# Kernel tuning notes

Measured on AMD Instinct MI355X. Metric: run time of the kernel, lower is better.

The kernel has to match this reference:

```python
import jax, jax.numpy as jnp
import numpy as np

N = 50000          # nodes
E = 800000         # edges
F_IN = 128         # num_node_features
H = 64             # hidden_channels
G = 64             # graphs in batch
C = 10             # num_classes
L_HID = 3          # num_hidden_layers
EPS = 1e-5


def setup_inputs() -> dict:
    key = jax.random.key(0)
    ks = jax.random.split(key, 16)
    x = jax.random.normal(ks[0], (N, F_IN), dtype=jnp.float32)
    edge_index = jax.random.randint(ks[1], (2, E), 0, N, dtype=jnp.int32)
    batch = jnp.sort(jax.random.randint(ks[2], (N,), 0, G, dtype=jnp.int32))
    s = 0.05
    W_in = jax.random.normal(ks[3], (F_IN, H), dtype=jnp.float32) * s
    b_in = jnp.zeros((H,), dtype=jnp.float32)
    W_hid = jax.random.normal(ks[4], (L_HID, H, H), dtype=jnp.float32) * s
    b_hid = jnp.zeros((L_HID, H), dtype=jnp.float32)
    gamma = jnp.ones((H,), dtype=jnp.float32)
    beta = jnp.zeros((H,), dtype=jnp.float32)
    # MLPReadout: 64 -> 32 -> 16 -> 10
    W1 = jax.random.normal(ks[5], (H, H // 2), dtype=jnp.float32) * s
    b1 = jnp.zeros((H // 2,), dtype=jnp.float32)
    W2 = jax.random.normal(ks[6], (H // 2, H // 4), dtype=jnp.float32) * s
    b2 = jnp.zeros((H // 4,), dtype=jnp.float32)
    W3 = jax.random.normal(ks[7], (H // 4, C), dtype=jnp.float32) * s
    b3 = jnp.zeros((C,), dtype=jnp.float32)
    return {"x": x, "edge_index": edge_index, "batch": batch,
            "W_in": W_in, "b_in": b_in, "W_hid": W_hid, "b_hid": b_hid,
            "gamma": gamma, "beta": beta,
            "W1": W1, "b1": b1, "W2": W2, "b2": b2, "W3": W3, "b3": b3}


def gcn_conv(h_pre, W, b, src, dst, dis):
    # PyG GCNConv with self-loops: out_i = sum_{j->i} d_i^-.5 d_j^-.5 (x_j W) + d_i^-1 (x_i W) + b
    h = h_pre @ W                                   # [N, H]
    norm = (dis[src] * dis[dst])[:, None]           # [E, 1]
    agg = jax.ops.segment_sum(h[src] * norm, dst, num_segments=N)
    agg = agg + h * (dis * dis)[:, None]            # self-loop term
    return agg + b


def batchnorm(x, gamma, beta):
    mu = jnp.mean(x, axis=0)
    var = jnp.mean(jnp.square(x - mu), axis=0)      # biased var (torch BN)
    return (x - mu) * jax.lax.rsqrt(var + EPS) * gamma + beta


def reference(x, edge_index, batch, W_in, b_in, W_hid, b_hid,
              gamma, beta, W1, b1, W2, b2, W3, b3):
    src, dst = edge_index[0], edge_index[1]
    # degree with self-loops (computed on target nodes)
    deg = jax.ops.segment_sum(jnp.ones((E,), x.dtype), dst, num_segments=N) + 1.0
    dis = jax.lax.rsqrt(deg)                        # deg^-0.5

    h = jax.nn.relu(gcn_conv(x, W_in, b_in, src, dst, dis))
    for l in range(L_HID):
        h = gcn_conv(h, W_hid[l], b_hid[l], src, dst, dis)
        h = batchnorm(h, gamma, beta)
        h = jax.nn.relu(h)

    # global mean pool over graphs
    sums = jax.ops.segment_sum(h, batch, num_segments=G)           # [G, H]
    cnts = jax.ops.segment_sum(jnp.ones((N,), x.dtype), batch, num_segments=G)
    pooled = sums / jnp.maximum(cnts, 1.0)[:, None]

    # MLPReadout
    y = jax.nn.relu(pooled @ W1 + b1)
    y = jax.nn.relu(y @ W2 + b2)
    return y @ W3 + b3                               # [G, C]
```

## Files before the change

kernel.cpp:

```cpp
#include <hip/hip_runtime.h>

#define NN 50000
#define NE 800000
#define FIN 128
#define H 64
#define NG 64
#define NC 10
#define EPS 1e-5f
#define NB_SCAN 196
#define GATHER_BLOCKS 12500
#define BNRED_BLOCKS 125

__global__ void count_deg_kernel(const int* __restrict__ dst, int* __restrict__ deg) {
    int e = blockIdx.x * blockDim.x + threadIdx.x;
    if (e < NE) atomicAdd(&deg[dst[e]], 1);
}

__global__ void scan1_kernel(const int* __restrict__ deg, int* __restrict__ ebase,
                             int* __restrict__ bsum, float* __restrict__ dis) {
    __shared__ int s[256];
    int t = threadIdx.x;
    int i = blockIdx.x * 256 + t;
    int v = (i < NN) ? deg[i] : 0;
    if (i < NN) dis[i] = rsqrtf((float)v + 1.0f);
    s[t] = v;
    for (int off = 1; off < 256; off <<= 1) {
        __syncthreads();
        int add = (t >= off) ? s[t - off] : 0;
        __syncthreads();
        s[t] += add;
    }
    __syncthreads();
    if (i < NN) ebase[i] = s[t] - v;
    if (t == 255) bsum[blockIdx.x] = s[255];
}

__global__ void scan2_kernel(int* __restrict__ bsum, const int* __restrict__ batch,
                             int* __restrict__ gstart) {
    int t = threadIdx.x;
    if (t <= NG) {
        int lo = 0, hi = NN;
        while (lo < hi) {
            int mid = (lo + hi) >> 1;
            if (batch[mid] < t) lo = mid + 1; else hi = mid;
        }
        gstart[t] = lo;
    }
    __shared__ int s[256];
    int v = (t < NB_SCAN) ? bsum[t] : 0;
    s[t] = v;
    for (int off = 1; off < 256; off <<= 1) {
        __syncthreads();
        int add = (t >= off) ? s[t - off] : 0;
        __syncthreads();
        s[t] += add;
    }
    __syncthreads();
    if (t < NB_SCAN) bsum[t] = s[t] - v;
}

__global__ void scan3_kernel(int* __restrict__ ebase, const int* __restrict__ bsum) {
    int i = blockIdx.x * blockDim.x + threadIdx.x;
    if (i < NN) ebase[i] += bsum[i >> 8];
    if (i == 0) ebase[NN] = NE;
}

__global__ void fill_kernel(const int* __restrict__ src, const int* __restrict__ dst,
                            const int* __restrict__ ebase, int* __restrict__ cursor,
                            int* __restrict__ eidx) {
    int e = blockIdx.x * blockDim.x + threadIdx.x;
    if (e < NE) {
        int d = dst[e];
        int slot = ebase[d] + atomicAdd(&cursor[d], 1);
        eidx[slot] = src[e];
    }
}

__global__ __launch_bounds__(256, 4) void gemm_fin_kernel(const float* __restrict__ A,
                                                          const float* __restrict__ W,
                                                          const float* __restrict__ dis,
                                                          float* __restrict__ outp) {
    __shared__ float Al[64][65];
    __shared__ float Wl[64 * H];
    const int tid = threadIdx.x;
    const int r0 = blockIdx.x * 64;
    const int row = tid >> 2;
    const int cb  = (tid & 3) << 4;
    float acc[16];
#pragma unroll
    for (int j = 0; j < 16; j++) acc[j] = 0.f;

    for (int k0 = 0; k0 < FIN; k0 += 64) {
        for (int idx = tid; idx < 64 * H; idx += 256) Wl[idx] = W[k0 * H + idx];
        for (int idx = tid; idx < 64 * 64; idx += 256) {
            int r = idx >> 6, c = idx & 63;
            int gr = r0 + r;
            Al[r][c] = (gr < NN) ? A[(long)gr * FIN + k0 + c] : 0.f;
        }
        __syncthreads();
#pragma unroll
        for (int k = 0; k < 64; k++) {
            float a = Al[row][k];
#pragma unroll
            for (int j = 0; j < 16; j++) acc[j] = fmaf(a, Wl[k * H + cb + j], acc[j]);
        }
        __syncthreads();
    }
    int gr = r0 + row;
    if (gr < NN) {
        float ds = dis[gr];
#pragma unroll
        for (int j = 0; j < 16; j++) acc[j] *= ds;
        float4* o = reinterpret_cast<float4*>(&outp[(long)gr * H + cb]);
        o[0] = make_float4(acc[0], acc[1], acc[2], acc[3]);
        o[1] = make_float4(acc[4], acc[5], acc[6], acc[7]);
        o[2] = make_float4(acc[8], acc[9], acc[10], acc[11]);
        o[3] = make_float4(acc[12], acc[13], acc[14], acc[15]);
    }
}

template <int DO_BN>
__global__ __launch_bounds__(256, 4) void gemm_hid_kernel(const float* __restrict__ A,
                                                          const float* __restrict__ W,
                                                          const float* __restrict__ pbn2,
                                                          const float* __restrict__ gamma,
                                                          const float* __restrict__ beta,
                                                          const float* __restrict__ dis,
                                                          float* __restrict__ outp) {
    __shared__ float Al[64][65];
    __shared__ float Wl[64 * H];
    __shared__ float bns[128];
    __shared__ float tot[128];
    const int tid = threadIdx.x;
    if (DO_BN) {
        if (tid < 128) {
            float s = 0.f;
            for (int r = 0; r < BNRED_BLOCKS; ++r) s += pbn2[(long)r * 128 + tid];
            tot[tid] = s;
        }
        __syncthreads();
        if (tid < H) {
            float mu  = tot[tid] * (1.0f / NN);
            float var = tot[H + tid] * (1.0f / NN) - mu * mu;
            float sc  = rsqrtf(var + EPS) * gamma[tid];
            bns[tid]     = sc;
            bns[H + tid] = beta[tid] - mu * sc;
        }
        __syncthreads();
    }
    const int r0 = blockIdx.x * 64;
    const int row = tid >> 2;
    const int cb  = (tid & 3) << 4;
    float acc[16];
#pragma unroll
    for (int j = 0; j < 16; j++) acc[j] = 0.f;

    for (int idx = tid; idx < 64 * H; idx += 256) Wl[idx] = W[idx];
    for (int idx = tid; idx < 64 * 64; idx += 256) {
        int r = idx >> 6, c = idx & 63;
        int gr = r0 + r;
        float a = (gr < NN) ? A[(long)gr * H + c] : 0.f;
        if (DO_BN) a = fmaxf(fmaf(a, bns[c], bns[64 + c]), 0.f);
        Al[r][c] = a;
    }
    __syncthreads();
#pragma unroll
    for (int k = 0; k < 64; k++) {
        float a = Al[row][k];
#pragma unroll
        for (int j = 0; j < 16; j++) acc[j] = fmaf(a, Wl[k * H + cb + j], acc[j]);
    }
    int gr = r0 + row;
    if (gr < NN) {
        float ds = dis[gr];
#pragma unroll
        for (int j = 0; j < 16; j++) acc[j] *= ds;
        float4* o = reinterpret_cast<float4*>(&outp[(long)gr * H + cb]);
        o[0] = make_float4(acc[0], acc[1], acc[2], acc[3]);
        o[1] = make_float4(acc[4], acc[5], acc[6], acc[7]);
        o[2] = make_float4(acc[8], acc[9], acc[10], acc[11]);
        o[3] = make_float4(acc[12], acc[13], acc[14], acc[15]);
    }
}

template <int MODE>
__global__ __launch_bounds__(256) void gather_kernel(const float* __restrict__ hw,
                                                     const int* __restrict__ ebase,
                                                     const int* __restrict__ eidx,
                                                     const float* __restrict__ dis,
                                                     const float* __restrict__ bias,
                                                     float* __restrict__ outp,
                                                     float* __restrict__ pbn) {
    __shared__ float ls[H], lss[H];
    if (MODE == 1) {
        if (threadIdx.x < H) { ls[threadIdx.x] = 0.f; lss[threadIdx.x] = 0.f; }
        __syncthreads();
    }
    const int node = blockIdx.x * 4 + (threadIdx.x >> 6);
    const int lane = threadIdx.x & 63;
    const int grp  = lane >> 4;
    const int c4   = (lane & 15) << 2;
    const int e0 = ebase[node], e1 = ebase[node + 1];
    float4 acc = make_float4(0.f, 0.f, 0.f, 0.f);
    int e = e0 + grp;
    for (; e + 4 < e1; e += 8) {
        int s0 = eidx[e], s1 = eidx[e + 4];
        const float4 v0 = *reinterpret_cast<const float4*>(&hw[(long)s0 * H + c4]);
        const float4 v1 = *reinterpret_cast<const float4*>(&hw[(long)s1 * H + c4]);
        acc.x += v0.x + v1.x;
        acc.y += v0.y + v1.y;
        acc.z += v0.z + v1.z;
        acc.w += v0.w + v1.w;
    }
    if (e < e1) {
        const float4 v0 = *reinterpret_cast<const float4*>(&hw[(long)eidx[e] * H + c4]);
        acc.x += v0.x; acc.y += v0.y; acc.z += v0.z; acc.w += v0.w;
    }
#pragma unroll
    for (int m = 16; m <= 32; m <<= 1) {
        acc.x += __shfl_xor(acc.x, m, 64);
        acc.y += __shfl_xor(acc.y, m, 64);
        acc.z += __shfl_xor(acc.z, m, 64);
        acc.w += __shfl_xor(acc.w, m, 64);
    }
    const float4 self = *reinterpret_cast<const float4*>(&hw[(long)node * H + c4]);
    float ds = dis[node];
    float4 v;
    v.x = fmaf(acc.x + self.x, ds, bias[c4 + 0]);
    v.y = fmaf(acc.y + self.y, ds, bias[c4 + 1]);
    v.z = fmaf(acc.z + self.z, ds, bias[c4 + 2]);
    v.w = fmaf(acc.w + self.w, ds, bias[c4 + 3]);
    if (MODE == 0) {
        v.x = fmaxf(v.x, 0.f); v.y = fmaxf(v.y, 0.f);
        v.z = fmaxf(v.z, 0.f); v.w = fmaxf(v.w, 0.f);
    }
    if (grp == 0) {
        *reinterpret_cast<float4*>(&outp[(long)node * H + c4]) = v;
        if (MODE == 1) {
            atomicAdd(&ls[c4 + 0], v.x); atomicAdd(&lss[c4 + 0], v.x * v.x);
            atomicAdd(&ls[c4 + 1], v.y); atomicAdd(&lss[c4 + 1], v.y * v.y);
            atomicAdd(&ls[c4 + 2], v.z); atomicAdd(&lss[c4 + 2], v.z * v.z);
            atomicAdd(&ls[c4 + 3], v.w); atomicAdd(&lss[c4 + 3], v.w * v.w);
        }
    }
    if (MODE == 1) {
        __syncthreads();
        if (threadIdx.x < H) {
            pbn[(long)blockIdx.x * 128 + threadIdx.x] = ls[threadIdx.x];
            pbn[(long)blockIdx.x * 128 + H + threadIdx.x] = lss[threadIdx.x];
        }
    }
}

__global__ void bnredA_kernel(const float* __restrict__ pbn, float* __restrict__ pbn2) {
    int c = threadIdx.x & 127;
    int half = threadIdx.x >> 7;
    int r0 = blockIdx.x * 100;
    float s = 0.f;
    for (int r = r0 + half; r < r0 + 100; r += 2) s += pbn[(long)r * 128 + c];
    __shared__ float red[256];
    red[threadIdx.x] = s;
    __syncthreads();
    if (half == 0) pbn2[(long)blockIdx.x * 128 + c] = red[c] + red[128 + c];
}

__global__ void pool_mlp_kernel(const float* __restrict__ conv, const float* __restrict__ pbn2,
                                const float* __restrict__ gamma, const float* __restrict__ beta,
                                const int* __restrict__ gstart,
                                const float* __restrict__ W1, const float* __restrict__ b1,
                                const float* __restrict__ W2, const float* __restrict__ b2,
                                const float* __restrict__ W3, const float* __restrict__ b3,
                                float* __restrict__ out) {
    __shared__ float tot[128];
    __shared__ float bns[128];
    __shared__ float red[256];
    __shared__ float pl[H], y1[32], y2[16];
    const int t = threadIdx.x;
    const int g = blockIdx.x;
    if (t < 128) {
        float s = 0.f;
        for (int r = 0; r < BNRED_BLOCKS; ++r) s += pbn2[(long)r * 128 + t];
        tot[t] = s;
    }
    __syncthreads();
    if (t < H) {
        float mu  = tot[t] * (1.0f / NN);
        float var = tot[H + t] * (1.0f / NN) - mu * mu;
        float sc  = rsqrtf(var + EPS) * gamma[t];
        bns[t]     = sc;
        bns[H + t] = beta[t] - mu * sc;
    }
    __syncthreads();
    const int n0 = gstart[g], n1 = gstart[g + 1];
    const int sub = t >> 6, lane = t & 63;
    float sc = bns[lane], sh = bns[H + lane];
    float s = 0.f;
    for (int n = n0 + sub; n < n1; n += 4)
        s += fmaxf(fmaf(conv[(long)n * H + lane], sc, sh), 0.f);
    red[t] = s;
    __syncthreads();
    if (sub == 0) {
        float inv = 1.0f / fmaxf((float)(n1 - n0), 1.0f);
        pl[lane] = (red[lane] + red[64 + lane] + red[128 + lane] + red[192 + lane]) * inv;
    }
    __syncthreads();
    if (t < 32) {
        float v = b1[t];
        for (int k = 0; k < H; k++) v = fmaf(pl[k], W1[k * 32 + t], v);
        y1[t] = fmaxf(v, 0.f);
    }
    __syncthreads();
    if (t < 16) {
        float v = b2[t];
        for (int k = 0; k < 32; k++) v = fmaf(y1[k], W2[k * 16 + t], v);
        y2[t] = fmaxf(v, 0.f);
    }
    __syncthreads();
    if (t < NC) {
        float v = b3[t];
        for (int k = 0; k < 16; k++) v = fmaf(y2[k], W3[k * NC + t], v);
        out[(long)g * NC + t] = v;
    }
}

extern "C" void kernel_launch(void* const* d_in, const int* in_sizes, int n_in,
                              void* d_out, int out_size, void* d_ws, size_t ws_size,
                              hipStream_t stream) {
    const float* x     = (const float*)d_in[0];
    const int*   ei    = (const int*)d_in[1];
    const int*   batch = (const int*)d_in[2];
    const float* W_in  = (const float*)d_in[3];
    const float* b_in  = (const float*)d_in[4];
    const float* W_hid = (const float*)d_in[5];
    const float* b_hid = (const float*)d_in[6];
    const float* gamma = (const float*)d_in[7];
    const float* beta  = (const float*)d_in[8];
    const float* W1    = (const float*)d_in[9];
    const float* b1    = (const float*)d_in[10];
    const float* W2    = (const float*)d_in[11];
    const float* b2    = (const float*)d_in[12];
    const float* W3    = (const float*)d_in[13];
    const float* b3    = (const float*)d_in[14];
    float* out = (float*)d_out;

    const int* src = ei;
    const int* dst = ei + NE;

    int*   deg_i  = (int*)d_ws;
    int*   cursor = deg_i + 50048;
    int*   ebase  = cursor + 50048;
    int*   eidx   = ebase + 50056;
    int*   bsum   = eidx + 800000;
    int*   gstart = bsum + 256;
    float* dis    = (float*)(gstart + 72);
    float* hw     = dis + 50048;
    float* conv   = hw + (long)NN * H;
    float* h      = conv + (long)NN * H;
    float* pbn    = h + (long)NN * H;
    float* pbn2   = pbn + (long)GATHER_BLOCKS * 128;

    const int NB_GEMM = (NN + 63) / 64;
    const int NB_E    = (NE + 255) / 256;
    const int NB_N    = (NN + 255) / 256;

    hipMemsetAsync(deg_i, 0, 2 * 50048 * sizeof(int), stream);
    count_deg_kernel<<<NB_E, 256, 0, stream>>>(dst, deg_i);
    scan1_kernel<<<NB_SCAN, 256, 0, stream>>>(deg_i, ebase, bsum, dis);
    scan2_kernel<<<1, 256, 0, stream>>>(bsum, batch, gstart);
    scan3_kernel<<<NB_N, 256, 0, stream>>>(ebase, bsum);
    fill_kernel<<<NB_E, 256, 0, stream>>>(src, dst, ebase, cursor, eidx);

    gemm_fin_kernel<<<NB_GEMM, 256, 0, stream>>>(x, W_in, dis, hw);
    gather_kernel<0><<<GATHER_BLOCKS, 256, 0, stream>>>(hw, ebase, eidx, dis, b_in, h, nullptr);

    gemm_hid_kernel<0><<<NB_GEMM, 256, 0, stream>>>(h, W_hid, nullptr, nullptr, nullptr, dis, hw);
    gather_kernel<1><<<GATHER_BLOCKS, 256, 0, stream>>>(hw, ebase, eidx, dis, b_hid, conv, pbn);
    bnredA_kernel<<<BNRED_BLOCKS, 256, 0, stream>>>(pbn, pbn2);
    for (int l = 1; l < 3; l++) {
        gemm_hid_kernel<1><<<NB_GEMM, 256, 0, stream>>>(conv, W_hid + (long)l * H * H, pbn2,
                                                        gamma, beta, dis, hw);
        gather_kernel<1><<<GATHER_BLOCKS, 256, 0, stream>>>(hw, ebase, eidx, dis,
                                                            b_hid + (long)l * H, conv, pbn);
        bnredA_kernel<<<BNRED_BLOCKS, 256, 0, stream>>>(pbn, pbn2);
    }

    pool_mlp_kernel<<<NG, 256, 0, stream>>>(conv, pbn2, gamma, beta, gstart,
                                            W1, b1, W2, b2, W3, b3, out);
}
```

Before: 609.7 us.

## Vectorize GEMM tile loads, deepen gather unroll, hoist BN stats, split pooling

GEMM kernels now load the A and W tiles with float4 reads instead of scalar loads. The gather loop is unrolled to four neighbour loads per iteration so more memory requests are in flight. The BatchNorm scale and shift are now computed once per layer in a small bnredB kernel, replacing the 125-row reduction that every GEMM block and every pooling block repeated. Pooling is split across 8 blocks per graph with a second kernel for the MLP, adding launches in exchange for more parallelism.

```diff
diff --git a/kernel.cpp b/kernel.cpp
--- a/kernel.cpp
+++ b/kernel.cpp
@@ -91,11 +91,17 @@
     for (int j = 0; j < 16; j++) acc[j] = 0.f;
 
     for (int k0 = 0; k0 < FIN; k0 += 64) {
-        for (int idx = tid; idx < 64 * H; idx += 256) Wl[idx] = W[k0 * H + idx];
-        for (int idx = tid; idx < 64 * 64; idx += 256) {
-            int r = idx >> 6, c = idx & 63;
+        for (int idx = tid; idx < 64 * 16; idx += 256) {
+            float4 w = *reinterpret_cast<const float4*>(&W[k0 * H + idx * 4]);
+            *reinterpret_cast<float4*>(&Wl[idx * 4]) = w;
+        }
+        for (int idx = tid; idx < 64 * 16; idx += 256) {
+            int r = idx >> 4, c4 = (idx & 15) << 2;
             int gr = r0 + r;
-            Al[r][c] = (gr < NN) ? A[(long)gr * FIN + k0 + c] : 0.f;
+            float4 a = make_float4(0.f, 0.f, 0.f, 0.f);
+            if (gr < NN) a = *reinterpret_cast<const float4*>(&A[(long)gr * FIN + k0 + c4]);
+            Al[r][c4 + 0] = a.x; Al[r][c4 + 1] = a.y;
+            Al[r][c4 + 2] = a.z; Al[r][c4 + 3] = a.w;
         }
         __syncthreads();
 #pragma unroll
@@ -122,30 +128,15 @@
 template <int DO_BN>
 __global__ __launch_bounds__(256, 4) void gemm_hid_kernel(const float* __restrict__ A,
                                                           const float* __restrict__ W,
-                                                          const float* __restrict__ pbn2,
-                                                          const float* __restrict__ gamma,
-                                                          const float* __restrict__ beta,
+                                                          const float* __restrict__ bnsc,
                                                           const float* __restrict__ dis,
                                                           float* __restrict__ outp) {
     __shared__ float Al[64][65];
     __shared__ float Wl[64 * H];
     __shared__ float bns[128];
-    __shared__ float tot[128];
     const int tid = threadIdx.x;
     if (DO_BN) {
-        if (tid < 128) {
-            float s = 0.f;
-            for (int r = 0; r < BNRED_BLOCKS; ++r) s += pbn2[(long)r * 128 + tid];
-            tot[tid] = s;
-        }
-        __syncthreads();
-        if (tid < H) {
-            float mu  = tot[tid] * (1.0f / NN);
-            float var = tot[H + tid] * (1.0f / NN) - mu * mu;
-            float sc  = rsqrtf(var + EPS) * gamma[tid];
-            bns[tid]     = sc;
-            bns[H + tid] = beta[tid] - mu * sc;
-        }
+        if (tid < 128) bns[tid] = bnsc[tid];
         __syncthreads();
     }
     const int r0 = blockIdx.x * 64;
@@ -155,13 +146,23 @@
 #pragma unroll
     for (int j = 0; j < 16; j++) acc[j] = 0.f;
 
-    for (int idx = tid; idx < 64 * H; idx += 256) Wl[idx] = W[idx];
-    for (int idx = tid; idx < 64 * 64; idx += 256) {
-        int r = idx >> 6, c = idx & 63;
+    for (int idx = tid; idx < 64 * 16; idx += 256) {
+        float4 w = *reinterpret_cast<const float4*>(&W[idx * 4]);
+        *reinterpret_cast<float4*>(&Wl[idx * 4]) = w;
+    }
+    for (int idx = tid; idx < 64 * 16; idx += 256) {
+        int r = idx >> 4, c4 = (idx & 15) << 2;
         int gr = r0 + r;
-        float a = (gr < NN) ? A[(long)gr * H + c] : 0.f;
-        if (DO_BN) a = fmaxf(fmaf(a, bns[c], bns[64 + c]), 0.f);
-        Al[r][c] = a;
+        float4 a = make_float4(0.f, 0.f, 0.f, 0.f);
+        if (gr < NN) a = *reinterpret_cast<const float4*>(&A[(long)gr * H + c4]);
+        if (DO_BN) {
+            a.x = fmaxf(fmaf(a.x, bns[c4 + 0], bns[64 + c4 + 0]), 0.f);
+            a.y = fmaxf(fmaf(a.y, bns[c4 + 1], bns[64 + c4 + 1]), 0.f);
+            a.z = fmaxf(fmaf(a.z, bns[c4 + 2], bns[64 + c4 + 2]), 0.f);
+            a.w = fmaxf(fmaf(a.w, bns[c4 + 3], bns[64 + c4 + 3]), 0.f);
+        }
+        Al[r][c4 + 0] = a.x; Al[r][c4 + 1] = a.y;
+        Al[r][c4 + 2] = a.z; Al[r][c4 + 3] = a.w;
     }
     __syncthreads();
 #pragma unroll
@@ -203,16 +204,18 @@
     const int e0 = ebase[node], e1 = ebase[node + 1];
     float4 acc = make_float4(0.f, 0.f, 0.f, 0.f);
     int e = e0 + grp;
-    for (; e + 4 < e1; e += 8) {
-        int s0 = eidx[e], s1 = eidx[e + 4];
+    for (; e + 12 < e1; e += 16) {
+        int s0 = eidx[e], s1 = eidx[e + 4], s2 = eidx[e + 8], s3 = eidx[e + 12];
         const float4 v0 = *reinterpret_cast<const float4*>(&hw[(long)s0 * H + c4]);
         const float4 v1 = *reinterpret_cast<const float4*>(&hw[(long)s1 * H + c4]);
-        acc.x += v0.x + v1.x;
-        acc.y += v0.y + v1.y;
-        acc.z += v0.z + v1.z;
-        acc.w += v0.w + v1.w;
-    }
-    if (e < e1) {
+        const float4 v2 = *reinterpret_cast<const float4*>(&hw[(long)s2 * H + c4]);
+        const float4 v3 = *reinterpret_cast<const float4*>(&hw[(long)s3 * H + c4]);
+        acc.x += (v0.x + v1.x) + (v2.x + v3.x);
+        acc.y += (v0.y + v1.y) + (v2.y + v3.y);
+        acc.z += (v0.z + v1.z) + (v2.z + v3.z);
+        acc.w += (v0.w + v1.w) + (v2.w + v3.w);
+    }
+    for (; e < e1; e += 4) {
         const float4 v0 = *reinterpret_cast<const float4*>(&hw[(long)eidx[e] * H + c4]);
         acc.x += v0.x; acc.y += v0.y; acc.z += v0.z; acc.w += v0.w;
     }
@@ -264,45 +267,53 @@
     if (half == 0) pbn2[(long)blockIdx.x * 128 + c] = red[c] + red[128 + c];
 }
 
-__global__ void pool_mlp_kernel(const float* __restrict__ conv, const float* __restrict__ pbn2,
-                                const float* __restrict__ gamma, const float* __restrict__ beta,
-                                const int* __restrict__ gstart,
-                                const float* __restrict__ W1, const float* __restrict__ b1,
-                                const float* __restrict__ W2, const float* __restrict__ b2,
-                                const float* __restrict__ W3, const float* __restrict__ b3,
-                                float* __restrict__ out) {
+__global__ void bnredB_kernel(const float* __restrict__ pbn2, const float* __restrict__ gamma,
+                              const float* __restrict__ beta, float* __restrict__ bnsc) {
     __shared__ float tot[128];
-    __shared__ float bns[128];
-    __shared__ float red[256];
-    __shared__ float pl[H], y1[32], y2[16];
-    const int t = threadIdx.x;
-    const int g = blockIdx.x;
-    if (t < 128) {
-        float s = 0.f;
-        for (int r = 0; r < BNRED_BLOCKS; ++r) s += pbn2[(long)r * 128 + t];
-        tot[t] = s;
-    }
+    int t = threadIdx.x;
+    float s = 0.f;
+    for (int r = 0; r < BNRED_BLOCKS; ++r) s += pbn2[(long)r * 128 + t];
+    tot[t] = s;
     __syncthreads();
     if (t < H) {
         float mu  = tot[t] * (1.0f / NN);
         float var = tot[H + t] * (1.0f / NN) - mu * mu;
         float sc  = rsqrtf(var + EPS) * gamma[t];
-        bns[t]     = sc;
-        bns[H + t] = beta[t] - mu * sc;
-    }
-    __syncthreads();
+        bnsc[t]     = sc;
+        bnsc[H + t] = beta[t] - mu * sc;
+    }
+}
+
+__global__ __launch_bounds__(256) void poolA_kernel(const float* __restrict__ conv,
+                                                    const float* __restrict__ bnsc,
+                                                    const int* __restrict__ gstart,
+                                                    float* __restrict__ psum) {
+    const int g = blockIdx.x >> 3, s = blockIdx.x & 7;
     const int n0 = gstart[g], n1 = gstart[g + 1];
-    const int sub = t >> 6, lane = t & 63;
-    float sc = bns[lane], sh = bns[H + lane];
+    const int wave = threadIdx.x >> 6, lane = threadIdx.x & 63;
+    const float sc = bnsc[lane], sh = bnsc[H + lane];
+    float acc = 0.f;
+    for (int n = n0 + s + 8 * wave; n < n1; n += 32)
+        acc += fmaxf(fmaf(conv[(long)n * H + lane], sc, sh), 0.f);
+    __shared__ float red[256];
+    red[threadIdx.x] = acc;
+    __syncthreads();
+    if (wave == 0)
+        psum[(long)blockIdx.x * H + lane] = red[lane] + red[64 + lane] + red[128 + lane] + red[192 + lane];
+}
+
+__global__ void poolB_mlp_kernel(const float* __restrict__ psum, const int* __restrict__ gstart,
+                                 const float* __restrict__ W1, const float* __restrict__ b1,
+                                 const float* __restrict__ W2, const float* __restrict__ b2,
+                                 const float* __restrict__ W3, const float* __restrict__ b3,
+                                 float* __restrict__ out) {
+    __shared__ float pl[H], y1[32], y2[16];
+    const int g = blockIdx.x, t = threadIdx.x;
     float s = 0.f;
-    for (int n = n0 + sub; n < n1; n += 4)
-        s += fmaxf(fmaf(conv[(long)n * H + lane], sc, sh), 0.f);
-    red[t] = s;
-    __syncthreads();
-    if (sub == 0) {
-        float inv = 1.0f / fmaxf((float)(n1 - n0), 1.0f);
-        pl[lane] = (red[lane] + red[64 + lane] + red[128 + lane] + red[192 + lane]) * inv;
-    }
+#pragma unroll
+    for (int k = 0; k < 8; k++) s += psum[(long)(g * 8 + k) * H + t];
+    const int n0 = gstart[g], n1 = gstart[g + 1];
+    pl[t] = s / fmaxf((float)(n1 - n0), 1.0f);
     __syncthreads();
     if (t < 32) {
         float v = b1[t];
@@ -358,6 +369,8 @@
     float* h      = conv + (long)NN * H;
     float* pbn    = h + (long)NN * H;
     float* pbn2   = pbn + (long)GATHER_BLOCKS * 128;
+    float* bnsc   = pbn2 + BNRED_BLOCKS * 128;
+    float* psum   = bnsc + 128;
 
     const int NB_GEMM = (NN + 63) / 64;
     const int NB_E    = (NE + 255) / 256;
@@ -373,17 +386,18 @@
     gemm_fin_kernel<<<NB_GEMM, 256, 0, stream>>>(x, W_in, dis, hw);
     gather_kernel<0><<<GATHER_BLOCKS, 256, 0, stream>>>(hw, ebase, eidx, dis, b_in, h, nullptr);
 
-    gemm_hid_kernel<0><<<NB_GEMM, 256, 0, stream>>>(h, W_hid, nullptr, nullptr, nullptr, dis, hw);
+    gemm_hid_kernel<0><<<NB_GEMM, 256, 0, stream>>>(h, W_hid, nullptr, dis, hw);
     gather_kernel<1><<<GATHER_BLOCKS, 256, 0, stream>>>(hw, ebase, eidx, dis, b_hid, conv, pbn);
     bnredA_kernel<<<BNRED_BLOCKS, 256, 0, stream>>>(pbn, pbn2);
+    bnredB_kernel<<<1, 128, 0, stream>>>(pbn2, gamma, beta, bnsc);
     for (int l = 1; l < 3; l++) {
-        gemm_hid_kernel<1><<<NB_GEMM, 256, 0, stream>>>(conv, W_hid + (long)l * H * H, pbn2,
-                                                        gamma, beta, dis, hw);
+        gemm_hid_kernel<1><<<NB_GEMM, 256, 0, stream>>>(conv, W_hid + (long)l * H * H, bnsc, dis, hw);
         gather_kernel<1><<<GATHER_BLOCKS, 256, 0, stream>>>(hw, ebase, eidx, dis,
                                                             b_hid + (long)l * H, conv, pbn);
         bnredA_kernel<<<BNRED_BLOCKS, 256, 0, stream>>>(pbn, pbn2);
-    }
-
-    pool_mlp_kernel<<<NG, 256, 0, stream>>>(conv, pbn2, gamma, beta, gstart,
-                                            W1, b1, W2, b2, W3, b3, out);
-}
+        bnredB_kernel<<<1, 128, 0, stream>>>(pbn2, gamma, beta, bnsc);
+    }
+
+    poolA_kernel<<<NG * 8, 256, 0, stream>>>(conv, bnsc, gstart, psum);
+    poolB_mlp_kernel<<<NG, 64, 0, stream>>>(psum, gstart, W1, b1, W2, b2, W3, b3, out);
+}
```

Measured after the change: 553.7 us. 9.2% less time.
